# Optimization experiments

Measured on AMD Instinct MI355X. Metric: run time of the kernel, lower is better.

The kernel has to match this reference:

```python
import jax, jax.numpy as jnp
import numpy as np

B, H, K, NUM_PTR, MAX_LEN = 32768, 896, 2000, 2, 128


def setup_inputs() -> dict:
    key = jax.random.key(0)
    k1, k2, k3 = jax.random.split(key, 3)
    z = jax.random.normal(k1, (B, H), dtype=jnp.float32)
    # codebook init: normal(0, 0.02) as in torch.nn.init.normal_
    emb = 0.02 * jax.random.normal(k2, (K, H), dtype=jnp.float32)
    # pointer heads: two Linear(H, MAX_LEN) layers, stacked
    W = jax.random.normal(k3, (NUM_PTR, MAX_LEN, H), dtype=jnp.float32) / np.float32(np.sqrt(H))
    b = jnp.zeros((NUM_PTR, MAX_LEN), dtype=jnp.float32)
    return {"z": z, "emb": emb, "W": W, "b": b, "prompt_len": 96}


def reference(z, emb, W, b, prompt_len):
    # --- quantize: L2 cdist + argmin + gather + straight-through ---
    # dist[b,k] = ||z_b||^2 - 2 z_b . e_k + ||e_k||^2   -> [B, K]
    dist = (jnp.sum(z * z, axis=1, keepdims=True)
            - 2.0 * (z @ emb.T)
            + jnp.sum(emb * emb, axis=1)[None, :])
    idx = jnp.argmin(dist, axis=1)            # [B]
    z_q = emb[idx]                            # [B, H]
    op_state = z + jax.lax.stop_gradient(z_q - z)
    # --- pointer heads with prompt-length mask ---
    logits = jnp.einsum('bh,plh->bpl', z, W) + b[None, :, :]   # [B, 2, MAX_LEN]
    mask = jnp.where(jnp.arange(logits.shape[-1]) < prompt_len, 0.0, -jnp.inf)
    ptr_logits = logits + mask[None, None, :]
    return op_state, ptr_logits
```

## Files before the change

### kernel.cpp

```cpp
#include <hip/hip_runtime.h>
#include <hip/hip_bf16.h>
#include <cstdint>
#include <cstddef>

#define B_SZ 32768
#define H_SZ 896
#define K_SZ 2000
#define KPAD 2048
#define NPTR_COLS 256
#define NCAT 2304
#define BM 256
#define BN 256
#define BK 32
#define NKS (H_SZ / BK)
#define NT_ARG 8

typedef float floatx4 __attribute__((ext_vector_type(4)));
typedef __bf16 bf16x8 __attribute__((ext_vector_type(8)));

#define MASK_NEG 1.0e30f

__device__ inline unsigned short f2bf_rne(float x) {
  unsigned u = __builtin_bit_cast(unsigned, x);
  unsigned r = u + 0x7fffu + ((u >> 16) & 1u);
  return (unsigned short)(r >> 16);
}
__device__ inline float bf2f(unsigned short b) {
  unsigned u = ((unsigned)b) << 16;
  return __builtin_bit_cast(float, u);
}

typedef __attribute__((address_space(1))) void GV;
typedef __attribute__((address_space(3))) void LV;
__device__ inline void load_lds16(const void* gsrc, void* ldst) {
  __builtin_amdgcn_global_load_lds((GV*)gsrc, (LV*)ldst, 16, 0, 0);
}

__global__ __launch_bounds__(256) void convert_all(
    const float* __restrict__ emb, const float* __restrict__ W,
    const float* __restrict__ z,
    unsigned short* __restrict__ cat_hi, unsigned short* __restrict__ cat_lo,
    float* __restrict__ normE,
    unsigned short* __restrict__ zhi, unsigned short* __restrict__ zlo) {
  const int bid = blockIdx.x;
  const int tid = threadIdx.x;
  if (bid < NCAT) {
    const int row = bid;
    const float* src = nullptr;
    bool zero = false;
    if (row < K_SZ)       src = emb + (size_t)row * H_SZ;
    else if (row < KPAD)  zero = true;
    else                  src = W + (size_t)(row - KPAD) * H_SZ;

    float ss = 0.f;
    for (int c = tid; c < H_SZ; c += 256) {
      float x = zero ? 0.f : src[c];
      unsigned short hb = f2bf_rne(x);
      float hf = bf2f(hb);
      unsigned short lb = f2bf_rne(x - hf);
      cat_hi[(size_t)row * H_SZ + c] = hb;
      cat_lo[(size_t)row * H_SZ + c] = lb;
      ss += x * x;
    }
    #pragma unroll
    for (int off = 32; off > 0; off >>= 1) ss += __shfl_down(ss, off);
    __shared__ float wsum[4];
    const int wave = tid >> 6, lane = tid & 63;
    if (lane == 0) wsum[wave] = ss;
    __syncthreads();
    if (tid == 0 && row < KPAD) normE[row] = wsum[0] + wsum[1] + wsum[2] + wsum[3];
  } else {
    const size_t t = (size_t)(bid - NCAT) * 256 + tid;
    const float* src = z + t * 8;
    float x[8];
    *(float4*)&x[0] = *(const float4*)src;
    *(float4*)&x[4] = *(const float4*)(src + 4);
    unsigned hv[4], lv[4];
    #pragma unroll
    for (int q = 0; q < 4; ++q) {
      unsigned short h0 = f2bf_rne(x[2 * q]), h1 = f2bf_rne(x[2 * q + 1]);
      float r0 = x[2 * q] - bf2f(h0), r1 = x[2 * q + 1] - bf2f(h1);
      unsigned short l0 = f2bf_rne(r0), l1 = f2bf_rne(r1);
      hv[q] = (unsigned)h0 | ((unsigned)h1 << 16);
      lv[q] = (unsigned)l0 | ((unsigned)l1 << 16);
    }
    *(uint4*)(zhi + t * 8) = make_uint4(hv[0], hv[1], hv[2], hv[3]);
    *(uint4*)(zlo + t * 8) = make_uint4(lv[0], lv[1], lv[2], lv[3]);
  }
}

__global__ __launch_bounds__(512, 2) void main_gemm(
    const unsigned short* __restrict__ zhi,
    const unsigned short* __restrict__ zlo,
    const unsigned short* __restrict__ cat_hi,
    const unsigned short* __restrict__ cat_lo,
    const float* __restrict__ normE,
    const float* __restrict__ bias,
    const int* __restrict__ plen_p,
    float* __restrict__ pmin, int* __restrict__ pidx,
    float* __restrict__ out_logits) {
  __shared__ unsigned short ldsA[2][2][BM * BK];
  __shared__ unsigned short ldsB[2][2][BN * BK];
  __shared__ float red_v[4][BM];
  __shared__ int   red_i[4][BM];

  const int tid = threadIdx.x;
  const int wave = tid >> 6, lane = tid & 63;
  const int wm = wave >> 2, wn = wave & 3;
  const int m0 = blockIdx.x * BM;
  const int nt = blockIdx.y;
  const int n0 = nt * BN;
  const int lrow = lane & 15, lk = lane >> 4;
  const int csw = ((lk ^ ((lrow >> 1) & 3)) << 3);

  const int srow = lane >> 2;
  const int scol = (((lane & 3) ^ ((lane >> 3) & 3)) << 3);

  size_t offA[2], offB[2];
  #pragma unroll
  for (int s = 0; s < 2; ++s) {
    const int seg = wave * 2 + s;
    offA[s] = (size_t)(m0 + seg * 16 + srow) * H_SZ + scol;
    offB[s] = (size_t)(n0 + seg * 16 + srow) * H_SZ + scol;
  }

  auto STAGE = [&](int b, int s, int kk) {
    const int seg = wave * 2 + s;
    load_lds16(zhi    + offA[s] + kk, &ldsA[b][0][seg * 512]);
    load_lds16(zlo    + offA[s] + kk, &ldsA[b][1][seg * 512]);
    load_lds16(cat_hi + offB[s] + kk, &ldsB[b][0][seg * 512]);
    load_lds16(cat_lo + offB[s] + kk, &ldsB[b][1][seg * 512]);
  };

  floatx4 acc[8][4];
  #pragma unroll
  for (int i = 0; i < 8; ++i)
    #pragma unroll
    for (int j = 0; j < 4; ++j) acc[i][j] = (floatx4){0.f, 0.f, 0.f, 0.f};

  STAGE(0, 0, 0);
  STAGE(0, 1, 0);
  asm volatile("s_waitcnt vmcnt(0)" ::: "memory");
  __builtin_amdgcn_s_barrier();

  for (int ks = 0; ks < NKS; ++ks) {
    const int cur = ks & 1, nxt = cur ^ 1;
    const int kk1 = (ks + 1) * BK;
    const bool pf = (ks + 1 < NKS);

    bf16x8 a1h[4], a1l[4], a2h[4], a2l[4], bh[4], bl[4];

    #pragma unroll
    for (int i = 0; i < 4; ++i) {
      const int r = (wm * 128 + i * 16 + lrow) * BK + csw;
      a1h[i] = *(const bf16x8*)&ldsA[cur][0][r];
      a1l[i] = *(const bf16x8*)&ldsA[cur][1][r];
    }
    #pragma unroll
    for (int j = 0; j < 4; ++j) {
      const int r = (wn * 64 + j * 16 + lrow) * BK + csw;
      bh[j] = *(const bf16x8*)&ldsB[cur][0][r];
      bl[j] = *(const bf16x8*)&ldsB[cur][1][r];
    }
    if (pf) { STAGE(nxt, 0, kk1); STAGE(nxt, 1, kk1); }

    __builtin_amdgcn_s_setprio(1);
    #pragma unroll
    for (int i = 0; i < 4; ++i)
      #pragma unroll
      for (int j = 0; j < 2; ++j) {
        floatx4 c = acc[i][j];
        c = __builtin_amdgcn_mfma_f32_16x16x32_bf16(a1h[i], bh[j], c, 0, 0, 0);
        c = __builtin_amdgcn_mfma_f32_16x16x32_bf16(a1h[i], bl[j], c, 0, 0, 0);
        c = __builtin_amdgcn_mfma_f32_16x16x32_bf16(a1l[i], bh[j], c, 0, 0, 0);
        acc[i][j] = c;
      }
    #pragma unroll
    for (int i = 0; i < 4; ++i) {
      const int r = (wm * 128 + (4 + i) * 16 + lrow) * BK + csw;
      a2h[i] = *(const bf16x8*)&ldsA[cur][0][r];
      a2l[i] = *(const bf16x8*)&ldsA[cur][1][r];
    }
    #pragma unroll
    for (int i = 0; i < 4; ++i)
      #pragma unroll
      for (int j = 0; j < 2; ++j) {
        floatx4 c = acc[i][2 + j];
        c = __builtin_amdgcn_mfma_f32_16x16x32_bf16(a1h[i], bh[2 + j], c, 0, 0, 0);
        c = __builtin_amdgcn_mfma_f32_16x16x32_bf16(a1h[i], bl[2 + j], c, 0, 0, 0);
        c = __builtin_amdgcn_mfma_f32_16x16x32_bf16(a1l[i], bh[2 + j], c, 0, 0, 0);
        acc[i][2 + j] = c;
      }
    #pragma unroll
    for (int i = 0; i < 4; ++i)
      #pragma unroll
      for (int j = 0; j < 2; ++j) {
        floatx4 c = acc[4 + i][2 + j];
        c = __builtin_amdgcn_mfma_f32_16x16x32_bf16(a2h[i], bh[2 + j], c, 0, 0, 0);
        c = __builtin_amdgcn_mfma_f32_16x16x32_bf16(a2h[i], bl[2 + j], c, 0, 0, 0);
        c = __builtin_amdgcn_mfma_f32_16x16x32_bf16(a2l[i], bh[2 + j], c, 0, 0, 0);
        acc[4 + i][2 + j] = c;
      }
    #pragma unroll
    for (int i = 0; i < 4; ++i)
      #pragma unroll
      for (int j = 0; j < 2; ++j) {
        floatx4 c = acc[4 + i][j];
        c = __builtin_amdgcn_mfma_f32_16x16x32_bf16(a2h[i], bh[j], c, 0, 0, 0);
        c = __builtin_amdgcn_mfma_f32_16x16x32_bf16(a2h[i], bl[j], c, 0, 0, 0);
        c = __builtin_amdgcn_mfma_f32_16x16x32_bf16(a2l[i], bh[j], c, 0, 0, 0);
        acc[4 + i][j] = c;
      }
    __builtin_amdgcn_s_setprio(0);

    if (pf) { asm volatile("s_waitcnt vmcnt(0)" ::: "memory"); }
    __builtin_amdgcn_s_barrier();
    __builtin_amdgcn_sched_barrier(0);
  }

  if (nt < NT_ARG) {
    float nE[4]; bool valid[4]; int kcol[4];
    #pragma unroll
    for (int nj = 0; nj < 4; ++nj) {
      kcol[nj] = n0 + wn * 64 + nj * 16 + lrow;
      valid[nj] = (kcol[nj] < K_SZ);
      nE[nj] = normE[kcol[nj]];
    }
    #pragma unroll
    for (int mi = 0; mi < 8; ++mi) {
      #pragma unroll
      for (int r = 0; r < 4; ++r) {
        float v = 3.4e38f; int id = kcol[0];
        #pragma unroll
        for (int nj = 0; nj < 4; ++nj) {
          const float vv = valid[nj] ? (nE[nj] - 2.0f * acc[mi][nj][r]) : 3.4e38f;
          if (vv < v) { v = vv; id = kcol[nj]; }
        }
        #pragma unroll
        for (int m = 1; m < 16; m <<= 1) {
          const float ov = __shfl_xor(v, m);
          const int   oid = __shfl_xor(id, m);
          if (ov < v || (ov == v && oid < id)) { v = ov; id = oid; }
        }
        if (lrow == 0) {
          const int row_local = wm * 128 + mi * 16 + lk * 4 + r;
          red_v[wn][row_local] = v;
          red_i[wn][row_local] = id;
        }
      }
    }
    __syncthreads();
    if (tid < BM) {
      float v = red_v[0][tid]; int id = red_i[0][tid];
      #pragma unroll
      for (int w = 1; w < 4; ++w) {
        const float vw = red_v[w][tid];
        if (vw < v) { v = vw; id = red_i[w][tid]; }
      }
      pmin[(size_t)nt * B_SZ + m0 + tid] = v;
      pidx[(size_t)nt * B_SZ + m0 + tid] = id;
    }
  } else {
    const int plen = *plen_p;
    #pragma unroll
    for (int nj = 0; nj < 4; ++nj) {
      const int c = wn * 64 + nj * 16 + lrow;
      const float bv = bias[c];
      const bool masked = ((c & 127) >= plen);
      #pragma unroll
      for (int mi = 0; mi < 8; ++mi) {
        const int growbase = m0 + wm * 128 + mi * 16 + lk * 4;
        #pragma unroll
        for (int r = 0; r < 4; ++r) {
          const float val = masked ? -MASK_NEG : (acc[mi][nj][r] + bv);
          out_logits[(size_t)(growbase + r) * NPTR_COLS + c] = val;
        }
      }
    }
  }
}

__global__ __launch_bounds__(256) void merge_gather(
    const float* __restrict__ z, const float* __restrict__ emb,
    const float* __restrict__ pmin, const int* __restrict__ pidx,
    float* __restrict__ out0) {
  const int row = blockIdx.x;
  float v = pmin[row];
  int  id = pidx[row];
  #pragma unroll
  for (int t = 1; t < NT_ARG; ++t) {
    const float vt = pmin[(size_t)t * B_SZ + row];
    if (vt < v) { v = vt; id = pidx[(size_t)t * B_SZ + row]; }
  }
  const float4* e4 = (const float4*)(emb + (size_t)id * H_SZ);
  const float4* z4 = (const float4*)(z + (size_t)row * H_SZ);
  float4* o4 = (float4*)(out0 + (size_t)row * H_SZ);
  const int t = threadIdx.x;
  if (t < H_SZ / 4) {
    const float4 zz = z4[t], ee = e4[t];
    float4 r;
    r.x = zz.x + (ee.x - zz.x);
    r.y = zz.y + (ee.y - zz.y);
    r.z = zz.z + (ee.z - zz.z);
    r.w = zz.w + (ee.w - zz.w);
    o4[t] = r;
  }
}

extern "C" void kernel_launch(void* const* d_in, const int* in_sizes, int n_in,
                              void* d_out, int out_size, void* d_ws, size_t ws_size,
                              hipStream_t stream) {
  const float* z    = (const float*)d_in[0];
  const float* emb  = (const float*)d_in[1];
  const float* W    = (const float*)d_in[2];
  const float* bias = (const float*)d_in[3];
  const int*   plen = (const int*)d_in[4];
  float* out = (float*)d_out;

  char* ws = (char*)d_ws;
  unsigned short* cat_hi = (unsigned short*)(ws);
  unsigned short* cat_lo = (unsigned short*)(ws + 4128768);
  float* normE = (float*)(ws + 8257536);
  float* pmin  = (float*)(ws + 8265728);
  int*   pidx  = (int*)(ws + 9314304);

  unsigned short* zhi = (unsigned short*)out;
  unsigned short* zlo = zhi + (size_t)B_SZ * H_SZ;
  float* out_logits = out + (size_t)B_SZ * H_SZ;

  convert_all<<<dim3(NCAT + B_SZ * H_SZ / 2048), dim3(256), 0, stream>>>(
      emb, W, z, cat_hi, cat_lo, normE, zhi, zlo);
  main_gemm<<<dim3(B_SZ / BM, 9), dim3(512), 0, stream>>>(
      zhi, zlo, cat_hi, cat_lo, normE, bias, plen, pmin, pidx, out_logits);
  merge_gather<<<dim3(B_SZ), dim3(256), 0, stream>>>(z, emb, pmin, pidx, out);
}
```

Before: 669.9 us.

## Switch main GEMM to 32x32x16 MFMA with smaller 128x256x16 tiles

Shrinks the block tile from 256x256x32 to 128x256x16 and swaps the 16x16x32 MFMA for the 32x32x16 bf16 MFMA. Each wave now holds a 64x64 tile as 2x2 floatx16 accumulators, and the LDS staging and swizzle are rewritten to match. Launch bounds move to 4 blocks per CU for higher occupancy. The argmin and logits epilogues are remapped to the 32x32 accumulator layout. The trade-off is more A-tile reuse per block lost, twice as many K steps each with a barrier, and more global reloads of the codebook, against lower register pressure and more blocks in flight.

```diff
diff --git a/kernel.cpp b/kernel.cpp
--- a/kernel.cpp
+++ b/kernel.cpp
@@ -9,13 +9,14 @@
 #define KPAD 2048
 #define NPTR_COLS 256
 #define NCAT 2304
-#define BM 256
+#define BM 128
 #define BN 256
-#define BK 32
+#define BK 16
 #define NKS (H_SZ / BK)
 #define NT_ARG 8
 
 typedef float floatx4 __attribute__((ext_vector_type(4)));
+typedef float floatx16 __attribute__((ext_vector_type(16)));
 typedef __bf16 bf16x8 __attribute__((ext_vector_type(8)));
 
 #define MASK_NEG 1.0e30f
@@ -89,7 +90,7 @@
   }
 }
 
-__global__ __launch_bounds__(512, 2) void main_gemm(
+__global__ __launch_bounds__(512, 4) void main_gemm(
     const unsigned short* __restrict__ zhi,
     const unsigned short* __restrict__ zlo,
     const unsigned short* __restrict__ cat_hi,
@@ -110,36 +111,39 @@
   const int m0 = blockIdx.x * BM;
   const int nt = blockIdx.y;
   const int n0 = nt * BN;
-  const int lrow = lane & 15, lk = lane >> 4;
-  const int csw = ((lk ^ ((lrow >> 1) & 3)) << 3);
-
-  const int srow = lane >> 2;
-  const int scol = (((lane & 3) ^ ((lane >> 3) & 3)) << 3);
-
-  size_t offA[2], offB[2];
+  const int l31 = lane & 31, lh = lane >> 5;
+
+  const int srow = lane >> 1;
+  const int sslot = (lane & 1) ^ ((lane >> 3) & 1);
+  const int planeA = wave >> 2, cA = wave & 3;
+  const unsigned short* srcA =
+      (planeA ? zlo : zhi) + (size_t)(m0 + cA * 32 + srow) * H_SZ + sslot * 8;
+  const size_t goffB = (size_t)(n0 + wave * 32 + srow) * H_SZ + sslot * 8;
+  const unsigned short* srcBh = cat_hi + goffB;
+  const unsigned short* srcBl = cat_lo + goffB;
+
+  auto STAGE = [&](int b, int kk) {
+    load_lds16(srcA + kk,  &ldsA[b][planeA][cA * 512]);
+    load_lds16(srcBh + kk, &ldsB[b][0][wave * 512]);
+    load_lds16(srcBl + kk, &ldsB[b][1][wave * 512]);
+  };
+
+  floatx16 acc[2][2];
   #pragma unroll
-  for (int s = 0; s < 2; ++s) {
-    const int seg = wave * 2 + s;
-    offA[s] = (size_t)(m0 + seg * 16 + srow) * H_SZ + scol;
-    offB[s] = (size_t)(n0 + seg * 16 + srow) * H_SZ + scol;
-  }
-
-  auto STAGE = [&](int b, int s, int kk) {
-    const int seg = wave * 2 + s;
-    load_lds16(zhi    + offA[s] + kk, &ldsA[b][0][seg * 512]);
-    load_lds16(zlo    + offA[s] + kk, &ldsA[b][1][seg * 512]);
-    load_lds16(cat_hi + offB[s] + kk, &ldsB[b][0][seg * 512]);
-    load_lds16(cat_lo + offB[s] + kk, &ldsB[b][1][seg * 512]);
-  };
-
-  floatx4 acc[8][4];
+  for (int i = 0; i < 2; ++i)
+    #pragma unroll
+    for (int j = 0; j < 2; ++j) acc[i][j] = (floatx16)(0.f);
+
+  int adA[2], adB[2];
   #pragma unroll
-  for (int i = 0; i < 8; ++i)
-    #pragma unroll
-    for (int j = 0; j < 4; ++j) acc[i][j] = (floatx4){0.f, 0.f, 0.f, 0.f};
-
-  STAGE(0, 0, 0);
-  STAGE(0, 1, 0);
+  for (int t = 0; t < 2; ++t) {
+    const int ra = wm * 64 + t * 32 + l31;
+    adA[t] = ra * 16 + ((lh ^ ((ra >> 2) & 1)) << 3);
+    const int rb = wn * 64 + t * 32 + l31;
+    adB[t] = rb * 16 + ((lh ^ ((rb >> 2) & 1)) << 3);
+  }
+
+  STAGE(0, 0);
   asm volatile("s_waitcnt vmcnt(0)" ::: "memory");
   __builtin_amdgcn_s_barrier();
 
@@ -148,69 +152,37 @@
     const int kk1 = (ks + 1) * BK;
     const bool pf = (ks + 1 < NKS);
 
-    bf16x8 a1h[4], a1l[4], a2h[4], a2l[4], bh[4], bl[4];
-
-    #pragma unroll
-    for (int i = 0; i < 4; ++i) {
-      const int r = (wm * 128 + i * 16 + lrow) * BK + csw;
-      a1h[i] = *(const bf16x8*)&ldsA[cur][0][r];
-      a1l[i] = *(const bf16x8*)&ldsA[cur][1][r];
-    }
-    #pragma unroll
-    for (int j = 0; j < 4; ++j) {
-      const int r = (wn * 64 + j * 16 + lrow) * BK + csw;
-      bh[j] = *(const bf16x8*)&ldsB[cur][0][r];
-      bl[j] = *(const bf16x8*)&ldsB[cur][1][r];
-    }
-    if (pf) { STAGE(nxt, 0, kk1); STAGE(nxt, 1, kk1); }
+    bf16x8 ah[2], al[2], bh[2], bl[2];
+    #pragma unroll
+    for (int t = 0; t < 2; ++t) {
+      ah[t] = *(const bf16x8*)&ldsA[cur][0][adA[t]];
+      al[t] = *(const bf16x8*)&ldsA[cur][1][adA[t]];
+    }
+    bh[0] = *(const bf16x8*)&ldsB[cur][0][adB[0]];
+    bl[0] = *(const bf16x8*)&ldsB[cur][1][adB[0]];
+    if (pf) STAGE(nxt, kk1);
 
     __builtin_amdgcn_s_setprio(1);
     #pragma unroll
-    for (int i = 0; i < 4; ++i)
-      #pragma unroll
-      for (int j = 0; j < 2; ++j) {
-        floatx4 c = acc[i][j];
-        c = __builtin_amdgcn_mfma_f32_16x16x32_bf16(a1h[i], bh[j], c, 0, 0, 0);
-        c = __builtin_amdgcn_mfma_f32_16x16x32_bf16(a1h[i], bl[j], c, 0, 0, 0);
-        c = __builtin_amdgcn_mfma_f32_16x16x32_bf16(a1l[i], bh[j], c, 0, 0, 0);
-        acc[i][j] = c;
-      }
-    #pragma unroll
-    for (int i = 0; i < 4; ++i) {
-      const int r = (wm * 128 + (4 + i) * 16 + lrow) * BK + csw;
-      a2h[i] = *(const bf16x8*)&ldsA[cur][0][r];
-      a2l[i] = *(const bf16x8*)&ldsA[cur][1][r];
-    }
-    #pragma unroll
-    for (int i = 0; i < 4; ++i)
-      #pragma unroll
-      for (int j = 0; j < 2; ++j) {
-        floatx4 c = acc[i][2 + j];
-        c = __builtin_amdgcn_mfma_f32_16x16x32_bf16(a1h[i], bh[2 + j], c, 0, 0, 0);
-        c = __builtin_amdgcn_mfma_f32_16x16x32_bf16(a1h[i], bl[2 + j], c, 0, 0, 0);
-        c = __builtin_amdgcn_mfma_f32_16x16x32_bf16(a1l[i], bh[2 + j], c, 0, 0, 0);
-        acc[i][2 + j] = c;
-      }
-    #pragma unroll
-    for (int i = 0; i < 4; ++i)
-      #pragma unroll
-      for (int j = 0; j < 2; ++j) {
-        floatx4 c = acc[4 + i][2 + j];
-        c = __builtin_amdgcn_mfma_f32_16x16x32_bf16(a2h[i], bh[2 + j], c, 0, 0, 0);
-        c = __builtin_amdgcn_mfma_f32_16x16x32_bf16(a2h[i], bl[2 + j], c, 0, 0, 0);
-        c = __builtin_amdgcn_mfma_f32_16x16x32_bf16(a2l[i], bh[2 + j], c, 0, 0, 0);
-        acc[4 + i][2 + j] = c;
-      }
-    #pragma unroll
-    for (int i = 0; i < 4; ++i)
-      #pragma unroll
-      for (int j = 0; j < 2; ++j) {
-        floatx4 c = acc[4 + i][j];
-        c = __builtin_amdgcn_mfma_f32_16x16x32_bf16(a2h[i], bh[j], c, 0, 0, 0);
-        c = __builtin_amdgcn_mfma_f32_16x16x32_bf16(a2h[i], bl[j], c, 0, 0, 0);
-        c = __builtin_amdgcn_mfma_f32_16x16x32_bf16(a2l[i], bh[j], c, 0, 0, 0);
-        acc[4 + i][j] = c;
-      }
+    for (int tm = 0; tm < 2; ++tm) {
+      floatx16 c = acc[tm][0];
+      c = __builtin_amdgcn_mfma_f32_32x32x16_bf16(ah[tm], bh[0], c, 0, 0, 0);
+      c = __builtin_amdgcn_mfma_f32_32x32x16_bf16(ah[tm], bl[0], c, 0, 0, 0);
+      c = __builtin_amdgcn_mfma_f32_32x32x16_bf16(al[tm], bh[0], c, 0, 0, 0);
+      acc[tm][0] = c;
+    }
+    __builtin_amdgcn_s_setprio(0);
+    bh[1] = *(const bf16x8*)&ldsB[cur][0][adB[1]];
+    bl[1] = *(const bf16x8*)&ldsB[cur][1][adB[1]];
+    __builtin_amdgcn_s_setprio(1);
+    #pragma unroll
+    for (int tm = 0; tm < 2; ++tm) {
+      floatx16 c = acc[tm][1];
+      c = __builtin_amdgcn_mfma_f32_32x32x16_bf16(ah[tm], bh[1], c, 0, 0, 0);
+      c = __builtin_amdgcn_mfma_f32_32x32x16_bf16(ah[tm], bl[1], c, 0, 0, 0);
+      c = __builtin_amdgcn_mfma_f32_32x32x16_bf16(al[tm], bh[1], c, 0, 0, 0);
+      acc[tm][1] = c;
+    }
     __builtin_amdgcn_s_setprio(0);
 
     if (pf) { asm volatile("s_waitcnt vmcnt(0)" ::: "memory"); }
@@ -219,31 +191,31 @@
   }
 
   if (nt < NT_ARG) {
-    float nE[4]; bool valid[4]; int kcol[4];
-    #pragma unroll
-    for (int nj = 0; nj < 4; ++nj) {
-      kcol[nj] = n0 + wn * 64 + nj * 16 + lrow;
-      valid[nj] = (kcol[nj] < K_SZ);
-      nE[nj] = normE[kcol[nj]];
-    }
-    #pragma unroll
-    for (int mi = 0; mi < 8; ++mi) {
+    float nE[2]; bool valid[2]; int kc[2];
+    #pragma unroll
+    for (int tn = 0; tn < 2; ++tn) {
+      kc[tn] = n0 + wn * 64 + tn * 32 + l31;
+      valid[tn] = (kc[tn] < K_SZ);
+      nE[tn] = normE[kc[tn]];
+    }
+    #pragma unroll
+    for (int tm = 0; tm < 2; ++tm) {
       #pragma unroll
-      for (int r = 0; r < 4; ++r) {
-        float v = 3.4e38f; int id = kcol[0];
+      for (int r = 0; r < 16; ++r) {
+        float v = 3.4e38f; int id = 0;
         #pragma unroll
-        for (int nj = 0; nj < 4; ++nj) {
-          const float vv = valid[nj] ? (nE[nj] - 2.0f * acc[mi][nj][r]) : 3.4e38f;
-          if (vv < v) { v = vv; id = kcol[nj]; }
+        for (int tn = 0; tn < 2; ++tn) {
+          const float vv = valid[tn] ? (nE[tn] - 2.0f * acc[tm][tn][r]) : 3.4e38f;
+          if (vv < v) { v = vv; id = kc[tn]; }
         }
         #pragma unroll
-        for (int m = 1; m < 16; m <<= 1) {
+        for (int m = 1; m < 32; m <<= 1) {
           const float ov = __shfl_xor(v, m);
           const int   oid = __shfl_xor(id, m);
           if (ov < v || (ov == v && oid < id)) { v = ov; id = oid; }
         }
-        if (lrow == 0) {
-          const int row_local = wm * 128 + mi * 16 + lk * 4 + r;
+        if (l31 == 0) {
+          const int row_local = wm * 64 + tm * 32 + (r & 3) + 8 * (r >> 2) + 4 * lh;
           red_v[wn][row_local] = v;
           red_i[wn][row_local] = id;
         }
@@ -263,17 +235,17 @@
   } else {
     const int plen = *plen_p;
     #pragma unroll
-    for (int nj = 0; nj < 4; ++nj) {
-      const int c = wn * 64 + nj * 16 + lrow;
+    for (int tn = 0; tn < 2; ++tn) {
+      const int c = wn * 64 + tn * 32 + l31;
       const float bv = bias[c];
       const bool masked = ((c & 127) >= plen);
       #pragma unroll
-      for (int mi = 0; mi < 8; ++mi) {
-        const int growbase = m0 + wm * 128 + mi * 16 + lk * 4;
+      for (int tm = 0; tm < 2; ++tm) {
         #pragma unroll
-        for (int r = 0; r < 4; ++r) {
-          const float val = masked ? -MASK_NEG : (acc[mi][nj][r] + bv);
-          out_logits[(size_t)(growbase + r) * NPTR_COLS + c] = val;
+        for (int r = 0; r < 16; ++r) {
+          const int grow = m0 + wm * 64 + tm * 32 + (r & 3) + 8 * (r >> 2) + 4 * lh;
+          const float val = masked ? -MASK_NEG : (acc[tm][tn][r] + bv);
+          out_logits[(size_t)grow * NPTR_COLS + c] = val;
         }
       }
     }
```

Result: slower. 786.3 us (+17.4%).
